# Optimization experiments

Hardware: AMD Instinct MI355X
Metric: run time of the kernel (lower is better)

## Reference

```python
import jax, jax.numpy as jnp
import numpy as np

NX, NY, NZ = 256, 256, 64
M = 400000
NFEATS = 16
OFFSETS = [(dx, dy, dz) for dx in (-1, 0, 1) for dy in (-1, 0, 1) for dz in (-1, 0, 1)]


def setup_inputs() -> dict:
    key = jax.random.key(0)
    ks = jax.random.split(key, 24)
    # unique active voxel sites (submanifold conv assumes unique active coords)
    flat = jax.random.permutation(ks[0], NX * NY * NZ)[:M]
    x = (flat // (NY * NZ)).astype(jnp.int32)
    y = ((flat // NZ) % NY).astype(jnp.int32)
    z = (flat % NZ).astype(jnp.int32)
    indices = jnp.stack([jnp.zeros_like(x), x, y, z], axis=-1)  # [M,4] = (batch,x,y,z)
    # dense grid -> row lookup (row+1, 0 means empty); this is the spconv rulebook analogue
    table = jnp.zeros(NX * NY * NZ, jnp.int32).at[flat].set(jnp.arange(M, dtype=jnp.int32) + 1)
    s = 0.05
    def w(k, shape):
        return jax.random.normal(ks[k], shape, jnp.float32) * s
    return {
        "features": jax.random.normal(ks[1], (M, NFEATS), jnp.float32),
        "w1": w(2, (27, NFEATS, 64)), "b1": w(3, (64,)),
        "w2": w(4, (27, 64, 64)), "b2": w(5, (64,)),
        "w3": w(6, (27, 64, 64)), "b3": w(7, (64,)),
        "cw11": w(8, (64, 64, 5, 5)), "cb11": w(9, (64,)),
        "cw12": w(10, (64, 64, 5, 5)), "cb12": w(11, (64,)),
        "cpw1": w(12, (64, 64, 1, 1)), "cpb1": w(13, (64,)),
        "cw21": w(14, (3, 64, 5, 5)), "cb21": w(15, (3,)),
        "cw22": w(16, (3, 3, 5, 5)), "cb22": w(17, (3,)),
        "cpw2": w(18, (3, 64, 1, 1)), "cpb2": w(19, (3,)),
        "indices": indices,
        "table": table,
    }


def subm_conv3d(feats, xyz, table, w, b):
    # submanifold 3x3x3 conv: outputs only at active sites, gathering active neighbors
    acc = jnp.zeros((feats.shape[0], w.shape[-1]), feats.dtype)
    for k, (dx, dy, dz) in enumerate(OFFSETS):
        nx, ny, nz = xyz[:, 0] + dx, xyz[:, 1] + dy, xyz[:, 2] + dz
        valid = (nx >= 0) & (nx < NX) & (ny >= 0) & (ny < NY) & (nz >= 0) & (nz < NZ)
        flat = jnp.clip(nx * (NY * NZ) + ny * NZ + nz, 0, NX * NY * NZ - 1)
        rows = table[flat]  # [M], 0 == empty
        ok = valid & (rows > 0)
        nf = feats[jnp.where(ok, rows - 1, 0)] * ok[:, None].astype(feats.dtype)
        acc = acc + nf @ w[k]  # gather-GEMM-accumulate
    return acc + b


def conv2d(x, w, b, pad):
    y = jax.lax.conv_general_dilated(x, w, (1, 1), [(pad, pad), (pad, pad)],
                                     dimension_numbers=("NCHW", "OIHW", "NCHW"))
    return y + b[None, :, None, None]


def resblock(x, w1, b1, w2, b2, pw, pb):
    h = jax.nn.relu(conv2d(x, w1, b1, 2))
    h = conv2d(h, w2, b2, 2)
    return jax.nn.relu(h + conv2d(x, pw, pb, 0))


def reference(features, w1, b1, w2, b2, w3, b3,
              cw11, cb11, cw12, cb12, cpw1, cpb1,
              cw21, cb21, cw22, cb22, cpw2, cpb2,
              indices, table):
    xyz = indices[:, 1:]
    h = jax.nn.relu(subm_conv3d(features, xyz, table, w1, b1))
    h = jax.nn.relu(subm_conv3d(h, xyz, table, w2, b2))
    h = subm_conv3d(h, xyz, table, w3, b3)
    # scatter-max voxel -> BEV over z (batch_size = 1)
    seg = indices[:, 1] * NY + indices[:, 2]
    bev = jax.ops.segment_max(h, seg, num_segments=NX * NY)
    bev = jnp.where(jnp.isneginf(bev), 0.0, bev)  # torch_scatter fills empty with 0
    bev = bev.reshape(1, NX, NY, 64).transpose(0, 3, 1, 2)  # NCHW
    out = resblock(bev, cw11, cb11, cw12, cb12, cpw1, cpb1)
    out = resblock(out, cw21, cb21, cw22, cb22, cpw2, cpb2)
    return out.transpose(0, 2, 3, 1)  # [1, NX, NY, 3]
```

## Files before the change

### kernel.cpp

```cpp
#include <hip/hip_runtime.h>
#include <math.h>

#define NXD 256
#define NYD 256
#define NZD 64
#define NCELL (NXD*NYD)

typedef __bf16 bf16x8 __attribute__((ext_vector_type(8)));
typedef float f32x4 __attribute__((ext_vector_type(4)));

__global__ __launch_bounds__(64) void zero_k(int* p) { p[threadIdx.x] = 0; }

__global__ __launch_bounds__(256) void f2bf_k(const float* __restrict__ in,
                                              __bf16* __restrict__ out, int n) {
    int i = blockIdx.x * 256 + threadIdx.x;
    if (i < n) out[i] = (__bf16)in[i];
}

__global__ __launch_bounds__(256) void count_k(const int* __restrict__ table,
                                               int* __restrict__ partial) {
    __shared__ int red[4];
    int tid = threadIdx.x, lane = tid & 63, wid = tid >> 6;
    int4 v = *(const int4*)(table + blockIdx.x * 1024 + tid * 4);
    int c = (v.x > 0) + (v.y > 0) + (v.z > 0) + (v.w > 0);
    for (int d = 32; d; d >>= 1) c += __shfl_down(c, d, 64);
    if (lane == 0) red[wid] = c;
    __syncthreads();
    if (tid == 0) partial[blockIdx.x] = red[0] + red[1] + red[2] + red[3];
}

__global__ __launch_bounds__(1024) void scan_k(const int* __restrict__ partial,
                                               int* __restrict__ scanned) {
    __shared__ int wsum[16];
    int tid = threadIdx.x, lane = tid & 63, wid = tid >> 6;
    int4 v = ((const int4*)partial)[tid];
    int tot = v.x + v.y + v.z + v.w;
    int sc = tot;
    for (int d = 1; d < 64; d <<= 1) { int o = __shfl_up(sc, d, 64); if (lane >= d) sc += o; }
    if (lane == 63) wsum[wid] = sc;
    __syncthreads();
    int wbase = 0;
    for (int w = 0; w < 16; ++w) if (w < wid) wbase += wsum[w];
    int excl = wbase + sc - tot;
    int4 o4;
    o4.x = excl; o4.y = excl + v.x; o4.z = excl + v.x + v.y; o4.w = excl + v.x + v.y + v.z;
    ((int4*)scanned)[tid] = o4;
}

__global__ __launch_bounds__(256) void emit_k(const int* __restrict__ table,
        const int* __restrict__ scanned, int* __restrict__ table2,
        int* __restrict__ perm, int4* __restrict__ coords) {
    __shared__ int wsum[4];
    int tid = threadIdx.x, lane = tid & 63, wid = tid >> 6;
    int gbase = blockIdx.x * 1024 + tid * 4;
    int4 v = *(const int4*)(table + gbase);
    int vals[4] = {v.x, v.y, v.z, v.w};
    int c = (v.x > 0) + (v.y > 0) + (v.z > 0) + (v.w > 0);
    int sc = c;
    for (int d = 1; d < 64; d <<= 1) { int o = __shfl_up(sc, d, 64); if (lane >= d) sc += o; }
    if (lane == 63) wsum[wid] = sc;
    __syncthreads();
    int wbase = 0;
    for (int w = 0; w < 4; ++w) if (w < wid) wbase += wsum[w];
    int pos = scanned[blockIdx.x] + wbase + sc - c;
    int t2[4];
    #pragma unroll
    for (int j = 0; j < 4; ++j) {
        int flat = gbase + j;
        if (vals[j] > 0) {
            t2[j] = pos + 1;
            perm[pos] = vals[j] - 1;
            coords[pos] = make_int4(0, flat >> 14, (flat >> 6) & 255, flat & 63);
            ++pos;
        } else t2[j] = 0;
    }
    *(int4*)(table2 + gbase) = make_int4(t2[0], t2[1], t2[2], t2[3]);
}

__global__ __launch_bounds__(256) void remap_feat_k(const float* __restrict__ f,
        const int* __restrict__ perm, __bf16* __restrict__ out) {
    int p = blockIdx.x * 64 + (threadIdx.x >> 2);
    int j = threadIdx.x & 3;
    float4 v = ((const float4*)(f + (size_t)perm[p] * 16))[j];
    __bf16* dst = out + (size_t)p * 16 + j * 4;
    dst[0] = (__bf16)v.x; dst[1] = (__bf16)v.y; dst[2] = (__bf16)v.z; dst[3] = (__bf16)v.w;
}

template<int CIN, int KS>
__global__ __launch_bounds__(256) void frag_w_k(const float* __restrict__ w,
                                                __bf16* __restrict__ wtf) {
    int k = blockIdx.x;
    for (int idx = threadIdx.x; idx < 4 * KS * 512; idx += 256) {
        int j = idx & 7, l = (idx >> 3) & 63, f = idx >> 9;
        int ctg = f / KS, ks = f % KS;
        int co = ctg * 16 + (l & 15);
        int ci = ks * 32 + ((l >> 4) * 8) + j;
        float v = (ci < CIN) ? w[((size_t)k * CIN + ci) * 64 + co] : 0.f;
        wtf[((size_t)k * 4 * KS + f) * 512 + (idx & 511)] = (__bf16)v;
    }
}

__global__ __launch_bounds__(256) void frag_w16p_k(const float* __restrict__ w,
                                                   __bf16* __restrict__ wtf) {
    int kp = blockIdx.x;
    for (int idx = threadIdx.x; idx < 4 * 512; idx += 256) {
        int j = idx & 7, l = (idx >> 3) & 63, f = idx >> 9;
        int co = f * 16 + (l & 15);
        int lg = l >> 4;
        int k = 2 * kp + (lg >> 1);
        int ci = (lg & 1) * 8 + j;
        float v = (k < 27) ? w[((size_t)k * 16 + ci) * 64 + co] : 0.f;
        wtf[((size_t)kp * 4 + f) * 512 + (idx & 511)] = (__bf16)v;
    }
}

template<int CO, int COPAD>
__global__ __launch_bounds__(256) void transpose_cw_k(const float* __restrict__ w,
                                                      __bf16* __restrict__ wt) {
    int k = blockIdx.x;
    for (int idx = threadIdx.x; idx < COPAD * 64; idx += 256) {
        int ci = idx & 63, co = idx >> 6;
        float v = (co < CO) ? w[((size_t)co * 64 + ci) * 25 + k] : 0.f;
        wt[((size_t)k * COPAD + co) * 64 + ci] = (__bf16)v;
    }
}

template<int CIN, bool RELU>
__global__ __launch_bounds__(256) void subm_mfma_k(
        const __bf16* __restrict__ feats,
        const int4* __restrict__ coords,
        const int* __restrict__ table,
        const __bf16* __restrict__ wtf,
        const float* __restrict__ bias,
        __bf16* __restrict__ outp,
        const __bf16* __restrict__ zp) {
    constexpr int KS = (CIN == 64) ? 2 : 1;
    constexpr int PH = (CIN == 64) ? 27 : 14;
    __shared__ int rows_lds[28][128];

    const int tid = threadIdx.x, lane = tid & 63, wid = tid >> 6;
    const int ch = wid & 1, pg = wid >> 1;
    const int lr = lane & 15, lg = lane >> 4;
    const int p0 = blockIdx.x * 128;

    if (ch == 0) {
        int4 c4 = coords[p0 + pg * 64 + lane];
        const int px = c4.y, py = c4.z, pz = c4.w;
        #pragma unroll
        for (int k = 0; k < 27; ++k) {
            const int nx = px + k / 9 - 1, ny = py + (k / 3) % 3 - 1, nz = pz + k % 3 - 1;
            const bool v = ((unsigned)nx < NXD) & ((unsigned)ny < NYD) & ((unsigned)nz < NZD);
            rows_lds[k][pg * 64 + lane] = v ? table[(nx * NYD + ny) * NZD + nz] : 0;
        }
        rows_lds[27][pg * 64 + lane] = 0;
    }
    __syncthreads();

    f32x4 acc[4][2];
    #pragma unroll
    for (int ct = 0; ct < 2; ++ct) {
        float b = bias[ch * 32 + ct * 16 + lr];
        #pragma unroll
        for (int pt = 0; pt < 4; ++pt) acc[pt][ct] = f32x4{b, b, b, b};
    }

    auto RD = [&](int p, int (&r)[4]) {
        if (p < PH) {
            const int kk = (CIN == 64) ? p : (2 * p + (lg >> 1));
            #pragma unroll
            for (int pt = 0; pt < 4; ++pt)
                r[pt] = rows_lds[kk][pg * 64 + pt * 16 + lr];
        }
    };

    auto LOADK = [&](int p, bf16x8 (&a)[4][KS], bf16x8 (&w)[2][KS], int& sm,
                     const int (&rr)[4]) {
        #pragma unroll
        for (int ct = 0; ct < 2; ++ct)
            #pragma unroll
            for (int ks = 0; ks < KS; ++ks)
                w[ct][ks] = *(const bf16x8*)(wtf +
                    ((size_t)(p * 4 + ch * 2 + ct) * KS + ks) * 512 + lane * 8);
        sm = 0;
        #pragma unroll
        for (int pt = 0; pt < 4; ++pt) {
            int srow = rr[pt];
            unsigned long long bm = __ballot(srow != 0);
            if (bm) {
                sm |= 1 << pt;
                if (CIN == 64) {
                    const __bf16* ab = (srow > 0) ? feats + (size_t)(srow - 1) * 64 : zp;
                    #pragma unroll
                    for (int ks = 0; ks < KS; ++ks)
                        a[pt][ks] = *(const bf16x8*)(ab + ks * 32 + lg * 8);
                } else {
                    const __bf16* ab = (srow > 0)
                        ? feats + (size_t)(srow - 1) * 16 + (lg & 1) * 8 : zp;
                    a[pt][0] = *(const bf16x8*)ab;
                }
            }
        }
    };
    auto MMAK = [&](bf16x8 (&a)[4][KS], bf16x8 (&w)[2][KS], int sm) {
        __builtin_amdgcn_s_setprio(1);
        #pragma unroll
        for (int pt = 0; pt < 4; ++pt)
            if (sm & (1 << pt))
                #pragma unroll
                for (int ct = 0; ct < 2; ++ct)
                    #pragma unroll
                    for (int ks = 0; ks < KS; ++ks)
                        acc[pt][ct] = __builtin_amdgcn_mfma_f32_16x16x32_bf16(
                            a[pt][ks], w[ct][ks], acc[pt][ct], 0, 0, 0);
        __builtin_amdgcn_s_setprio(0);
    };

    bf16x8 aX[4][KS], wX[2][KS], aY[4][KS], wY[2][KS];
    int smX, smY;
    int rA[4], rB[4];
    RD(0, rA);
    RD(1, rB);
    LOADK(0, aX, wX, smX, rA);
    #pragma unroll 1
    for (int p = 0; p + 2 < PH; p += 2) {
        RD(p + 2, rA);
        LOADK(p + 1, aY, wY, smY, rB);
        MMAK(aX, wX, smX);
        RD(p + 3, rB);
        LOADK(p + 2, aX, wX, smX, rA);
        MMAK(aY, wY, smY);
    }
    if constexpr (PH & 1) {
        MMAK(aX, wX, smX);
    } else {
        LOADK(PH - 1, aY, wY, smY, rB);
        MMAK(aX, wX, smX);
        MMAK(aY, wY, smY);
    }

    #pragma unroll
    for (int pt = 0; pt < 4; ++pt)
        #pragma unroll
        for (int ct = 0; ct < 2; ++ct) {
            const int co = ch * 32 + ct * 16 + lr;
            #pragma unroll
            for (int r = 0; r < 4; ++r) {
                int p = p0 + pg * 64 + pt * 16 + lg * 4 + r;
                float v = acc[pt][ct][r];
                if (RELU) v = fmaxf(v, 0.f);
                outp[(size_t)p * 64 + co] = (__bf16)v;
            }
        }
}

__global__ __launch_bounds__(256) void bev_max_k(const __bf16* __restrict__ h,
        const int* __restrict__ table, __bf16* __restrict__ bev) {
    int cell = blockIdx.x * 4 + (threadIdx.x >> 6);
    int lane = threadIdx.x & 63;
    int r = table[cell * 64 + lane];
    float acc = -INFINITY;
    #pragma unroll 1
    for (int z = 0; z < 64; ++z) {
        int row = __shfl(r, z, 64);
        if (row > 0) acc = fmaxf(acc, (float)h[(size_t)(row - 1) * 64 + lane]);
    }
    bev[(size_t)cell * 64 + lane] = (__bf16)((acc == -INFINITY) ? 0.f : acc);
}

template<bool RELU, bool FUSE_PW>
__global__ __launch_bounds__(256) void conv5_mfma_k(
        const __bf16* __restrict__ in,
        const __bf16* __restrict__ wtc,
        const float* __restrict__ bias,
        const __bf16* __restrict__ xres,
        const __bf16* __restrict__ wpw,
        const float* __restrict__ bpw,
        __bf16* __restrict__ out) {
    __shared__ __bf16 halo[400 * 64];
    __shared__ __bf16 xt[256 * 64];

    const int tid = threadIdx.x;
    const int gx0 = (blockIdx.x & 15) * 16;
    const int gy0 = (blockIdx.x >> 4) * 16;

    for (int i = tid; i < 3200; i += 256) {
        int hp = i >> 3, ch = i & 7;
        int hy = hp / 20, hx = hp - hy * 20;
        int gy = gy0 - 2 + hy, gx = gx0 - 2 + hx;
        uint4 v = {0, 0, 0, 0};
        if (gy >= 0 && gy < NXD && gx >= 0 && gx < NYD)
            v = *(const uint4*)(in + (((size_t)(gy << 8) + gx) << 6) + ch * 8);
        *(uint4*)((char*)halo + hp * 128 + ((ch ^ (hp & 7)) << 4)) = v;
    }
    if (FUSE_PW) {
        for (int i = tid; i < 2048; i += 256) {
            int p = i >> 3, ch = i & 7;
            int gy = gy0 + (p >> 4), gx = gx0 + (p & 15);
            uint4 v = *(const uint4*)(xres + (((size_t)(gy << 8) + gx) << 6) + ch * 8);
            *(uint4*)((char*)xt + p * 128 + ((ch ^ (p & 7)) << 4)) = v;
        }
    }
    __syncthreads();

    const int lane = tid & 63, wid = tid >> 6;
    const int lr = lane & 15, lg = lane >> 4;
    const int co = wid * 16 + lr;

    f32x4 acc[16];
    {
        float b = bias[co] + (FUSE_PW ? bpw[co] : 0.f);
        #pragma unroll
        for (int pt = 0; pt < 16; ++pt) acc[pt] = f32x4{b, b, b, b};
    }

    #pragma unroll 1
    for (int k = 0; k < 25; ++k) {
        const int dy = k / 5, dx = k - dy * 5;
        const __bf16* wrow = wtc + ((size_t)k * 64 + co) * 64 + lg * 8;
        bf16x8 bf0 = *(const bf16x8*)wrow;
        bf16x8 bf1 = *(const bf16x8*)(wrow + 32);
        #pragma unroll
        for (int pt = 0; pt < 16; ++pt) {
            int hp = (pt + dy) * 20 + lr + dx;
            bf16x8 a0 = *(const bf16x8*)((char*)halo + hp * 128 + ((lg ^ (hp & 7)) << 4));
            bf16x8 a1 = *(const bf16x8*)((char*)halo + hp * 128 + (((4 + lg) ^ (hp & 7)) << 4));
            acc[pt] = __builtin_amdgcn_mfma_f32_16x16x32_bf16(a0, bf0, acc[pt], 0, 0, 0);
            acc[pt] = __builtin_amdgcn_mfma_f32_16x16x32_bf16(a1, bf1, acc[pt], 0, 0, 0);
        }
    }
    if (FUSE_PW) {
        const __bf16* wrow = wpw + (size_t)co * 64 + lg * 8;
        bf16x8 bf0 = *(const bf16x8*)wrow;
        bf16x8 bf1 = *(const bf16x8*)(wrow + 32);
        #pragma unroll
        for (int pt = 0; pt < 16; ++pt) {
            int p = pt * 16 + lr;
            bf16x8 a0 = *(const bf16x8*)((char*)xt + p * 128 + ((lg ^ (p & 7)) << 4));
            bf16x8 a1 = *(const bf16x8*)((char*)xt + p * 128 + (((4 + lg) ^ (p & 7)) << 4));
            acc[pt] = __builtin_amdgcn_mfma_f32_16x16x32_bf16(a0, bf0, acc[pt], 0, 0, 0);
            acc[pt] = __builtin_amdgcn_mfma_f32_16x16x32_bf16(a1, bf1, acc[pt], 0, 0, 0);
        }
    }

    #pragma unroll
    for (int pt = 0; pt < 16; ++pt) {
        int gy = gy0 + pt;
        #pragma unroll
        for (int r = 0; r < 4; ++r) {
            int gx = gx0 + lg * 4 + r;
            float v = acc[pt][r];
            if (RELU) v = fmaxf(v, 0.f);
            out[(((size_t)(gy << 8) + gx) << 6) + co] = (__bf16)v;
        }
    }
}

__global__ __launch_bounds__(256) void conv5_mfma3_k(
        const __bf16* __restrict__ in,
        const __bf16* __restrict__ wtc,
        const float* __restrict__ bias3,
        float* __restrict__ out) {
    __shared__ __bf16 halo[400 * 64];

    const int tid = threadIdx.x;
    const int gx0 = (blockIdx.x & 15) * 16;
    const int gy0 = (blockIdx.x >> 4) * 16;

    for (int i = tid; i < 3200; i += 256) {
        int hp = i >> 3, ch = i & 7;
        int hy = hp / 20, hx = hp - hy * 20;
        int gy = gy0 - 2 + hy, gx = gx0 - 2 + hx;
        uint4 v = {0, 0, 0, 0};
        if (gy >= 0 && gy < NXD && gx >= 0 && gx < NYD)
            v = *(const uint4*)(in + (((size_t)(gy << 8) + gx) << 6) + ch * 8);
        *(uint4*)((char*)halo + hp * 128 + ((ch ^ (hp & 7)) << 4)) = v;
    }
    __syncthreads();

    const int lane = tid & 63, wid = tid >> 6;
    const int lr = lane & 15, lg = lane >> 4;

    f32x4 acc[4];
    {
        float b = (lr < 3) ? bias3[lr] : 0.f;
        #pragma unroll
        for (int t = 0; t < 4; ++t) acc[t] = f32x4{b, b, b, b};
    }

    #pragma unroll 1
    for (int k = 0; k < 25; ++k) {
        const int dy = k / 5, dx = k - dy * 5;
        const __bf16* wrow = wtc + ((size_t)k * 16 + lr) * 64 + lg * 8;
        bf16x8 bf0 = *(const bf16x8*)wrow;
        bf16x8 bf1 = *(const bf16x8*)(wrow + 32);
        #pragma unroll
        for (int t = 0; t < 4; ++t) {
            int pt = wid * 4 + t;
            int hp = (pt + dy) * 20 + lr + dx;
            bf16x8 a0 = *(const bf16x8*)((char*)halo + hp * 128 + ((lg ^ (hp & 7)) << 4));
            bf16x8 a1 = *(const bf16x8*)((char*)halo + hp * 128 + (((4 + lg) ^ (hp & 7)) << 4));
            acc[t] = __builtin_amdgcn_mfma_f32_16x16x32_bf16(a0, bf0, acc[t], 0, 0, 0);
            acc[t] = __builtin_amdgcn_mfma_f32_16x16x32_bf16(a1, bf1, acc[t], 0, 0, 0);
        }
    }

    if (lr < 3) {
        #pragma unroll
        for (int t = 0; t < 4; ++t) {
            int gy = gy0 + wid * 4 + t;
            #pragma unroll
            for (int r = 0; r < 4; ++r) {
                int gx = gx0 + lg * 4 + r;
                out[(size_t)lr * NCELL + (gy << 8) + gx] = fmaxf(acc[t][r], 0.f);
            }
        }
    }
}

template<int CIN, int COB, bool RELU>
__global__ __launch_bounds__(256) void conv5_k(const float* __restrict__ in,
        const float* __restrict__ w, const float* __restrict__ bias,
        float* __restrict__ out) {
    __shared__ float tile[20][20];
    int tid = threadIdx.x;
    int tx = tid & 15, ty = tid >> 4;
    int gx0 = blockIdx.x * 16 - 2, gy0 = blockIdx.y * 16 - 2;
    int co_base = blockIdx.z * COB;
    float acc[COB];
    #pragma unroll
    for (int i = 0; i < COB; ++i) acc[i] = bias[co_base + i];

    #pragma unroll 1
    for (int ci = 0; ci < CIN; ++ci) {
        __syncthreads();
        for (int idx = tid; idx < 400; idx += 256) {
            int r = idx / 20, cc = idx % 20;
            int sy = gy0 + r, sx = gx0 + cc;
            float v = 0.f;
            if (sy >= 0 && sy < NXD && sx >= 0 && sx < NYD)
                v = in[(size_t)ci * NCELL + sy * NYD + sx];
            tile[r][cc] = v;
        }
        __syncthreads();
        const float* wrow = w + ((size_t)co_base * CIN + ci) * 25;
        #pragma unroll
        for (int dy = 0; dy < 5; ++dy)
        #pragma unroll
        for (int dx = 0; dx < 5; ++dx) {
            float iv = tile[ty + dy][tx + dx];
            #pragma unroll
            for (int co = 0; co < COB; ++co)
                acc[co] = fmaf(iv, wrow[(size_t)co * CIN * 25 + dy * 5 + dx], acc[co]);
        }
    }
    int gy = gy0 + 2 + ty, gx = gx0 + 2 + tx;
    #pragma unroll
    for (int co = 0; co < COB; ++co) {
        float v = acc[co];
        if (RELU) v = fmaxf(v, 0.f);
        out[(size_t)(co_base + co) * NCELL + gy * NYD + gx] = v;
    }
}

__global__ __launch_bounds__(256) void pw_final_k(const __bf16* __restrict__ x,
        const float* __restrict__ pw, const float* __restrict__ pb,
        const float* __restrict__ h2, float* __restrict__ out) {
    int pix = blockIdx.x * 256 + threadIdx.x;
    float acc[3];
    #pragma unroll
    for (int co = 0; co < 3; ++co) acc[co] = pb[co] + h2[(size_t)co * NCELL + pix];
    const bf16x8* xr = (const bf16x8*)(x + (size_t)pix * 64);
    #pragma unroll
    for (int j = 0; j < 8; ++j) {
        bf16x8 v8 = xr[j];
        #pragma unroll
        for (int e = 0; e < 8; ++e) {
            float v = (float)v8[e];
            int ci = j * 8 + e;
            #pragma unroll
            for (int co = 0; co < 3; ++co) acc[co] = fmaf(v, pw[co * 64 + ci], acc[co]);
        }
    }
    #pragma unroll
    for (int co = 0; co < 3; ++co) out[(size_t)pix * 3 + co] = fmaxf(acc[co], 0.f);
}

extern "C" void kernel_launch(void* const* d_in, const int* in_sizes, int n_in,
                              void* d_out, int out_size, void* d_ws, size_t ws_size,
                              hipStream_t stream) {
    const float* features = (const float*)d_in[0];
    const float* w1   = (const float*)d_in[1];
    const float* b1   = (const float*)d_in[2];
    const float* w2   = (const float*)d_in[3];
    const float* b2   = (const float*)d_in[4];
    const float* w3   = (const float*)d_in[5];
    const float* b3   = (const float*)d_in[6];
    const float* cw11 = (const float*)d_in[7];
    const float* cb11 = (const float*)d_in[8];
    const float* cw12 = (const float*)d_in[9];
    const float* cb12 = (const float*)d_in[10];
    const float* cpw1 = (const float*)d_in[11];
    const float* cpb1 = (const float*)d_in[12];
    const float* cw21 = (const float*)d_in[13];
    const float* cb21 = (const float*)d_in[14];
    const float* cw22 = (const float*)d_in[15];
    const float* cb22 = (const float*)d_in[16];
    const float* cpw2 = (const float*)d_in[17];
    const float* cpb2 = (const float*)d_in[18];
    const int* table   = (const int*)d_in[20];
    const int M = in_sizes[0] / 16;

    char* ws = (char*)d_ws;
    __bf16* A_bf    = (__bf16*)(ws);
    __bf16* B_bf    = (__bf16*)(ws +  51200000ull);
    __bf16* feat_s  = (__bf16*)(ws + 102400000ull);
    __bf16* C_bf    = (__bf16*)(ws + 102400000ull);
    int4*   coords  = (int4*)  (ws + 153600000ull);
    int*    table2  = (int*)   (ws + 160000000ull);
    int*    perm    = (int*)   (ws + 176777216ull);
    int*    partial = (int*)   (ws + 178377216ull);
    int*    scanned = (int*)   (ws + 178393600ull);
    __bf16* BEV     = (__bf16*)(ws + 204800000ull);
    __bf16* H1      = (__bf16*)(ws + 213188608ull);
    __bf16* T1      = (__bf16*)(ws + 221577216ull);
    float*  S1      = (float*) (ws + 229965824ull);
    float*  S2      = (float*) (ws + 230752256ull);
    __bf16* WTC11   = (__bf16*)(ws + 232534016ull);
    __bf16* WTC12   = (__bf16*)(ws + 232738816ull);
    __bf16* WTC21   = (__bf16*)(ws + 232943616ull);
    __bf16* WPW1    = (__bf16*)(ws + 232994816ull);
    __bf16* WTF1    = (__bf16*)(ws + 233003008ull);
    __bf16* WTF2    = (__bf16*)(ws + 233113600ull);
    __bf16* WTF3    = (__bf16*)(ws + 233334784ull);
    __bf16* ZP      = (__bf16*)(ws + 233555968ull);

    count_k<<<4096, 256, 0, stream>>>(table, partial);
    scan_k<<<1, 1024, 0, stream>>>(partial, scanned);
    emit_k<<<4096, 256, 0, stream>>>(table, scanned, table2, perm, coords);
    remap_feat_k<<<M / 64, 256, 0, stream>>>(features, perm, feat_s);

    zero_k<<<1, 64, 0, stream>>>((int*)ZP);
    f2bf_k<<<16, 256, 0, stream>>>(cpw1, WPW1, 4096);
    frag_w16p_k<<<14, 256, 0, stream>>>(w1, WTF1);
    frag_w_k<64, 2><<<27, 256, 0, stream>>>(w2, WTF2);
    frag_w_k<64, 2><<<27, 256, 0, stream>>>(w3, WTF3);
    transpose_cw_k<64, 64><<<25, 256, 0, stream>>>(cw11, WTC11);
    transpose_cw_k<64, 64><<<25, 256, 0, stream>>>(cw12, WTC12);
    transpose_cw_k<3, 16><<<25, 256, 0, stream>>>(cw21, WTC21);

    const int pblocks = M / 128;
    subm_mfma_k<16, true ><<<pblocks, 256, 0, stream>>>(feat_s, coords, table2, WTF1, b1, A_bf, ZP);
    subm_mfma_k<64, true ><<<pblocks, 256, 0, stream>>>(A_bf,   coords, table2, WTF2, b2, B_bf, ZP);
    subm_mfma_k<64, false><<<pblocks, 256, 0, stream>>>(B_bf,   coords, table2, WTF3, b3, C_bf, ZP);

    bev_max_k<<<NCELL / 4, 256, 0, stream>>>(C_bf, table2, BEV);

    conv5_mfma_k<true, false><<<256, 256, 0, stream>>>(BEV, WTC11, cb11, nullptr, nullptr, nullptr, H1);
    conv5_mfma_k<true, true ><<<256, 256, 0, stream>>>(H1, WTC12, cb12, BEV, WPW1, cpb1, T1);

    conv5_mfma3_k<<<256, 256, 0, stream>>>(T1, WTC21, cb21, S1);
    conv5_k<3, 3, false><<<dim3(16, 16, 1), 256, 0, stream>>>(S1, cw22, cb22, S2);
    pw_final_k<<<NCELL / 256, 256, 0, stream>>>(T1, cpw2, cpb2, S2, (float*)d_out);
}
```

Measured before the change: 585.6 us.

## Repartition subm conv waves over all channels and halve BEV conv tiles

The sparse conv kernel now gives each wave 32 points across all 64 output channels, instead of 64 points across 32 channels. This means each gathered neighbour row is loaded once per block rather than twice. Weights are loaded per offset and activations are prefetched through a three-stage rotating buffer. The 5x5 BEV conv kernels move from 16x16 to 8x16 output tiles with twice as many blocks, which cuts LDS use and spreads work over more CUs, at the cost of a larger halo overhead per output.

```diff
diff --git a/kernel.cpp b/kernel.cpp
--- a/kernel.cpp
+++ b/kernel.cpp
@@ -139,52 +139,37 @@
     __shared__ int rows_lds[28][128];
 
     const int tid = threadIdx.x, lane = tid & 63, wid = tid >> 6;
-    const int ch = wid & 1, pg = wid >> 1;
     const int lr = lane & 15, lg = lane >> 4;
     const int p0 = blockIdx.x * 128;
 
-    if (ch == 0) {
-        int4 c4 = coords[p0 + pg * 64 + lane];
+    if (wid < 2) {
+        int4 c4 = coords[p0 + wid * 64 + lane];
         const int px = c4.y, py = c4.z, pz = c4.w;
         #pragma unroll
         for (int k = 0; k < 27; ++k) {
             const int nx = px + k / 9 - 1, ny = py + (k / 3) % 3 - 1, nz = pz + k % 3 - 1;
             const bool v = ((unsigned)nx < NXD) & ((unsigned)ny < NYD) & ((unsigned)nz < NZD);
-            rows_lds[k][pg * 64 + lane] = v ? table[(nx * NYD + ny) * NZD + nz] : 0;
-        }
-        rows_lds[27][pg * 64 + lane] = 0;
+            rows_lds[k][wid * 64 + lane] = v ? table[(nx * NYD + ny) * NZD + nz] : 0;
+        }
+        rows_lds[27][wid * 64 + lane] = 0;
     }
     __syncthreads();
 
-    f32x4 acc[4][2];
-    #pragma unroll
-    for (int ct = 0; ct < 2; ++ct) {
-        float b = bias[ch * 32 + ct * 16 + lr];
-        #pragma unroll
-        for (int pt = 0; pt < 4; ++pt) acc[pt][ct] = f32x4{b, b, b, b};
-    }
-
-    auto RD = [&](int p, int (&r)[4]) {
-        if (p < PH) {
+    f32x4 acc[2][4];
+    #pragma unroll
+    for (int ct = 0; ct < 4; ++ct) {
+        float b = bias[ct * 16 + lr];
+        #pragma unroll
+        for (int pt = 0; pt < 2; ++pt) acc[pt][ct] = f32x4{b, b, b, b};
+    }
+
+    auto LOADA = [&](int p, bf16x8 (&a)[2][KS], int& sm) {
+        if (p >= PH) return;
+        sm = 0;
+        #pragma unroll
+        for (int pt = 0; pt < 2; ++pt) {
             const int kk = (CIN == 64) ? p : (2 * p + (lg >> 1));
-            #pragma unroll
-            for (int pt = 0; pt < 4; ++pt)
-                r[pt] = rows_lds[kk][pg * 64 + pt * 16 + lr];
-        }
-    };
-
-    auto LOADK = [&](int p, bf16x8 (&a)[4][KS], bf16x8 (&w)[2][KS], int& sm,
-                     const int (&rr)[4]) {
-        #pragma unroll
-        for (int ct = 0; ct < 2; ++ct)
-            #pragma unroll
-            for (int ks = 0; ks < KS; ++ks)
-                w[ct][ks] = *(const bf16x8*)(wtf +
-                    ((size_t)(p * 4 + ch * 2 + ct) * KS + ks) * 512 + lane * 8);
-        sm = 0;
-        #pragma unroll
-        for (int pt = 0; pt < 4; ++pt) {
-            int srow = rr[pt];
+            int srow = rows_lds[kk][wid * 32 + pt * 16 + lr];
             unsigned long long bm = __ballot(srow != 0);
             if (bm) {
                 sm |= 1 << pt;
@@ -201,13 +186,21 @@
             }
         }
     };
-    auto MMAK = [&](bf16x8 (&a)[4][KS], bf16x8 (&w)[2][KS], int sm) {
+    auto LOADW = [&](int p, bf16x8 (&w)[4][KS]) {
+        #pragma unroll
+        for (int ct = 0; ct < 4; ++ct)
+            #pragma unroll
+            for (int ks = 0; ks < KS; ++ks)
+                w[ct][ks] = *(const bf16x8*)(wtf +
+                    ((size_t)(p * 4 + ct) * KS + ks) * 512 + lane * 8);
+    };
+    auto MMAK = [&](bf16x8 (&a)[2][KS], bf16x8 (&w)[4][KS], int sm) {
         __builtin_amdgcn_s_setprio(1);
         #pragma unroll
-        for (int pt = 0; pt < 4; ++pt)
+        for (int pt = 0; pt < 2; ++pt)
             if (sm & (1 << pt))
                 #pragma unroll
-                for (int ct = 0; ct < 2; ++ct)
+                for (int ct = 0; ct < 4; ++ct)
                     #pragma unroll
                     for (int ks = 0; ks < KS; ++ks)
                         acc[pt][ct] = __builtin_amdgcn_mfma_f32_16x16x32_bf16(
@@ -215,37 +208,35 @@
         __builtin_amdgcn_s_setprio(0);
     };
 
-    bf16x8 aX[4][KS], wX[2][KS], aY[4][KS], wY[2][KS];
-    int smX, smY;
-    int rA[4], rB[4];
-    RD(0, rA);
-    RD(1, rB);
-    LOADK(0, aX, wX, smX, rA);
+    bf16x8 aX[2][KS], aY[2][KS], aZ[2][KS], wU[4][KS];
+    int smX = 0, smY = 0, smZ = 0;
+    LOADA(0, aX, smX);
+    LOADA(1, aY, smY);
     #pragma unroll 1
-    for (int p = 0; p + 2 < PH; p += 2) {
-        RD(p + 2, rA);
-        LOADK(p + 1, aY, wY, smY, rB);
-        MMAK(aX, wX, smX);
-        RD(p + 3, rB);
-        LOADK(p + 2, aX, wX, smX, rA);
-        MMAK(aY, wY, smY);
-    }
-    if constexpr (PH & 1) {
-        MMAK(aX, wX, smX);
-    } else {
-        LOADK(PH - 1, aY, wY, smY, rB);
-        MMAK(aX, wX, smX);
-        MMAK(aY, wY, smY);
-    }
-
-    #pragma unroll
-    for (int pt = 0; pt < 4; ++pt)
-        #pragma unroll
-        for (int ct = 0; ct < 2; ++ct) {
-            const int co = ch * 32 + ct * 16 + lr;
+    for (int p = 0; p < PH; p += 3) {
+        LOADW(p, wU);
+        LOADA(p + 2, aZ, smZ);
+        MMAK(aX, wU, smX);
+        if (p + 1 < PH) {
+            LOADW(p + 1, wU);
+            LOADA(p + 3, aX, smX);
+            MMAK(aY, wU, smY);
+        }
+        if (p + 2 < PH) {
+            LOADW(p + 2, wU);
+            LOADA(p + 4, aY, smY);
+            MMAK(aZ, wU, smZ);
+        }
+    }
+
+    #pragma unroll
+    for (int pt = 0; pt < 2; ++pt)
+        #pragma unroll
+        for (int ct = 0; ct < 4; ++ct) {
+            const int co = ct * 16 + lr;
             #pragma unroll
             for (int r = 0; r < 4; ++r) {
-                int p = p0 + pg * 64 + pt * 16 + lg * 4 + r;
+                int p = p0 + wid * 32 + pt * 16 + lg * 4 + r;
                 float v = acc[pt][ct][r];
                 if (RELU) v = fmaxf(v, 0.f);
                 outp[(size_t)p * 64 + co] = (__bf16)v;
@@ -276,14 +267,14 @@
         const __bf16* __restrict__ wpw,
         const float* __restrict__ bpw,
         __bf16* __restrict__ out) {
-    __shared__ __bf16 halo[400 * 64];
-    __shared__ __bf16 xt[256 * 64];
+    __shared__ __bf16 halo[240 * 64];
+    __shared__ __bf16 xt[128 * 64];
 
     const int tid = threadIdx.x;
     const int gx0 = (blockIdx.x & 15) * 16;
-    const int gy0 = (blockIdx.x >> 4) * 16;
-
-    for (int i = tid; i < 3200; i += 256) {
+    const int gy0 = (blockIdx.x >> 4) * 8;
+
+    for (int i = tid; i < 1920; i += 256) {
         int hp = i >> 3, ch = i & 7;
         int hy = hp / 20, hx = hp - hy * 20;
         int gy = gy0 - 2 + hy, gx = gx0 - 2 + hx;
@@ -293,7 +284,7 @@
         *(uint4*)((char*)halo + hp * 128 + ((ch ^ (hp & 7)) << 4)) = v;
     }
     if (FUSE_PW) {
-        for (int i = tid; i < 2048; i += 256) {
+        for (int i = tid; i < 1024; i += 256) {
             int p = i >> 3, ch = i & 7;
             int gy = gy0 + (p >> 4), gx = gx0 + (p & 15);
             uint4 v = *(const uint4*)(xres + (((size_t)(gy << 8) + gx) << 6) + ch * 8);
@@ -306,11 +297,11 @@
     const int lr = lane & 15, lg = lane >> 4;
     const int co = wid * 16 + lr;
 
-    f32x4 acc[16];
+    f32x4 acc[8];
     {
         float b = bias[co] + (FUSE_PW ? bpw[co] : 0.f);
         #pragma unroll
-        for (int pt = 0; pt < 16; ++pt) acc[pt] = f32x4{b, b, b, b};
+        for (int pt = 0; pt < 8; ++pt) acc[pt] = f32x4{b, b, b, b};
     }
 
     #pragma unroll 1
@@ -320,7 +311,7 @@
         bf16x8 bf0 = *(const bf16x8*)wrow;
         bf16x8 bf1 = *(const bf16x8*)(wrow + 32);
         #pragma unroll
-        for (int pt = 0; pt < 16; ++pt) {
+        for (int pt = 0; pt < 8; ++pt) {
             int hp = (pt + dy) * 20 + lr + dx;
             bf16x8 a0 = *(const bf16x8*)((char*)halo + hp * 128 + ((lg ^ (hp & 7)) << 4));
             bf16x8 a1 = *(const bf16x8*)((char*)halo + hp * 128 + (((4 + lg) ^ (hp & 7)) << 4));
@@ -333,7 +324,7 @@
         bf16x8 bf0 = *(const bf16x8*)wrow;
         bf16x8 bf1 = *(const bf16x8*)(wrow + 32);
         #pragma unroll
-        for (int pt = 0; pt < 16; ++pt) {
+        for (int pt = 0; pt < 8; ++pt) {
             int p = pt * 16 + lr;
             bf16x8 a0 = *(const bf16x8*)((char*)xt + p * 128 + ((lg ^ (p & 7)) << 4));
             bf16x8 a1 = *(const bf16x8*)((char*)xt + p * 128 + (((4 + lg) ^ (p & 7)) << 4));
@@ -343,7 +334,7 @@
     }
 
     #pragma unroll
-    for (int pt = 0; pt < 16; ++pt) {
+    for (int pt = 0; pt < 8; ++pt) {
         int gy = gy0 + pt;
         #pragma unroll
         for (int r = 0; r < 4; ++r) {
@@ -360,13 +351,13 @@
         const __bf16* __restrict__ wtc,
         const float* __restrict__ bias3,
         float* __restrict__ out) {
-    __shared__ __bf16 halo[400 * 64];
+    __shared__ __bf16 halo[240 * 64];
 
     const int tid = threadIdx.x;
     const int gx0 = (blockIdx.x & 15) * 16;
-    const int gy0 = (blockIdx.x >> 4) * 16;
-
-    for (int i = tid; i < 3200; i += 256) {
+    const int gy0 = (blockIdx.x >> 4) * 8;
+
+    for (int i = tid; i < 1920; i += 256) {
         int hp = i >> 3, ch = i & 7;
         int hy = hp / 20, hx = hp - hy * 20;
         int gy = gy0 - 2 + hy, gx = gx0 - 2 + hx;
@@ -380,11 +371,11 @@
     const int lane = tid & 63, wid = tid >> 6;
     const int lr = lane & 15, lg = lane >> 4;
 
-    f32x4 acc[4];
+    f32x4 acc[2];
     {
         float b = (lr < 3) ? bias3[lr] : 0.f;
         #pragma unroll
-        for (int t = 0; t < 4; ++t) acc[t] = f32x4{b, b, b, b};
+        for (int t = 0; t < 2; ++t) acc[t] = f32x4{b, b, b, b};
     }
 
     #pragma unroll 1
@@ -394,8 +385,8 @@
         bf16x8 bf0 = *(const bf16x8*)wrow;
         bf16x8 bf1 = *(const bf16x8*)(wrow + 32);
         #pragma unroll
-        for (int t = 0; t < 4; ++t) {
-            int pt = wid * 4 + t;
+        for (int t = 0; t < 2; ++t) {
+            int pt = wid * 2 + t;
             int hp = (pt + dy) * 20 + lr + dx;
             bf16x8 a0 = *(const bf16x8*)((char*)halo + hp * 128 + ((lg ^ (hp & 7)) << 4));
             bf16x8 a1 = *(const bf16x8*)((char*)halo + hp * 128 + (((4 + lg) ^ (hp & 7)) << 4));
@@ -406,8 +397,8 @@
 
     if (lr < 3) {
         #pragma unroll
-        for (int t = 0; t < 4; ++t) {
-            int gy = gy0 + wid * 4 + t;
+        for (int t = 0; t < 2; ++t) {
+            int gy = gy0 + wid * 2 + t;
             #pragma unroll
             for (int r = 0; r < 4; ++r) {
                 int gx = gx0 + lg * 4 + r;
@@ -555,10 +546,10 @@
 
     bev_max_k<<<NCELL / 4, 256, 0, stream>>>(C_bf, table2, BEV);
 
-    conv5_mfma_k<true, false><<<256, 256, 0, stream>>>(BEV, WTC11, cb11, nullptr, nullptr, nullptr, H1);
-    conv5_mfma_k<true, true ><<<256, 256, 0, stream>>>(H1, WTC12, cb12, BEV, WPW1, cpb1, T1);
-
-    conv5_mfma3_k<<<256, 256, 0, stream>>>(T1, WTC21, cb21, S1);
+    conv5_mfma_k<true, false><<<512, 256, 0, stream>>>(BEV, WTC11, cb11, nullptr, nullptr, nullptr, H1);
+    conv5_mfma_k<true, true ><<<512, 256, 0, stream>>>(H1, WTC12, cb12, BEV, WPW1, cpb1, T1);
+
+    conv5_mfma3_k<<<512, 256, 0, stream>>>(T1, WTC21, cb21, S1);
     conv5_k<3, 3, false><<<dim3(16, 16, 1), 256, 0, stream>>>(S1, cw22, cb22, S2);
     pw_final_k<<<NCELL / 256, 256, 0, stream>>>(T1, cpw2, cpb2, S2, (float*)d_out);
 }
```

Measured after the change: 549.7 us. 1.07x faster.
